# Optimization experiments

Hardware: AMD Instinct MI355X
Metric: run time of the kernel (lower is better)

The kernel has to match this reference:

```python
import jax, jax.numpy as jnp
import numpy as np

B, L, D, H, E, K = 1, 512, 512, 512, 32, 2

def setup_inputs() -> dict:
    key = jax.random.key(0)
    ks = jax.random.split(key, 6)
    x = jax.random.normal(ks[0], (B, L, D), dtype=jnp.float32)
    router_scale = 1.0 + 0.02 * jax.random.normal(ks[1], (D,), dtype=jnp.float32)
    router_logits_w = 0.02 * jax.random.normal(ks[2], (D, E), dtype=jnp.float32)
    gating_einsum = 0.02 * jax.random.normal(ks[3], (E, 2, H, D), dtype=jnp.float32)
    linear_w = 0.02 * jax.random.normal(ks[4], (E, H, D), dtype=jnp.float32)
    per_expert_scale = 1.0 + 0.02 * jax.random.normal(ks[5], (E,), dtype=jnp.float32)
    return {"x": x, "router_scale": router_scale, "router_logits_w": router_logits_w,
            "gating_einsum": gating_einsum, "linear_w": linear_w,
            "per_expert_scale": per_expert_scale}

def reference(x, router_scale, router_logits_w, gating_einsum, linear_w, per_expert_scale):
    d = x.shape[-1]
    n_experts = router_logits_w.shape[-1]
    # RMSNorm without scale (fp32)
    x32 = x.astype(jnp.float32)
    var = jnp.mean(jnp.square(x32), axis=-1, keepdims=True)
    router_input = x32 * jax.lax.rsqrt(var + 1e-6)
    root_size = jax.lax.rsqrt(jnp.asarray(d, dtype=router_input.dtype))
    router_input = router_input * root_size * router_scale.astype(router_input.dtype)
    logits = jnp.dot(router_input, router_logits_w).astype(jnp.float32)  # [B,L,E]
    probs = jax.nn.softmax(logits, axis=-1)
    _, top_k_indices = jax.lax.top_k(logits, K)  # [B,L,K]
    indicator = jax.nn.one_hot(top_k_indices, n_experts, dtype=probs.dtype).sum(axis=-2)
    gate_weights = indicator * probs
    renorm = jnp.sum(gate_weights, axis=-1, keepdims=True)
    renorm = jnp.where(renorm > 0.0, renorm, 1.0)
    weights = probs / renorm
    top_k_weights = jnp.take_along_axis(weights, top_k_indices, axis=-1)  # [B,L,K]
    output = jnp.zeros_like(x)
    for ki in range(K):  # small fixed k; faithful to source's per-slot gather
        expert_idx = top_k_indices[:, :, ki]          # [B,L] int32
        expert_w = top_k_weights[:, :, ki]            # [B,L]
        gate_params = gating_einsum[expert_idx]       # [B,L,2,H,D] -- the big gather
        lin_params = linear_w[expert_idx]             # [B,L,H,D]
        escale = per_expert_scale[expert_idx]         # [B,L]
        gate_0 = jnp.einsum('bld,blhd->blh', x, gate_params[:, :, 0])
        gate_1 = jnp.einsum('bld,blhd->blh', x, gate_params[:, :, 1])
        activated = jax.nn.gelu(gate_0) * gate_1
        expert_out = jnp.einsum('blh,blhd->bld', activated, lin_params)
        output = output + expert_out * (escale * expert_w)[..., None]
    return output
```

## Files before the change

### kernel.cpp

```cpp
#include <hip/hip_runtime.h>
#include <hip/hip_bf16.h>
#include <math.h>

#define LTOK 512
#define DDIM 512
#define NEXP 32
#define HDIM 512

typedef __attribute__((ext_vector_type(8))) short short8;
typedef __attribute__((ext_vector_type(4))) float floatx4;

__device__ __forceinline__ unsigned bpack(float a, float b) {
    unsigned ua = __float_as_uint(a), ub = __float_as_uint(b);
    ua += 0x7FFFu + ((ua >> 16) & 1u);
    ub += 0x7FFFu + ((ub >> 16) & 1u);
    return (ua >> 16) | (ub & 0xFFFF0000u);
}


__global__ __launch_bounds__(64) void router_kernel(
    const float* __restrict__ x, const float* __restrict__ rs,
    const float* __restrict__ Wr, const float* __restrict__ pes,
    int* __restrict__ easgn, float* __restrict__ wts,
    short* __restrict__ xb, float* __restrict__ out)
{
    const int t = blockIdx.x;
    const int lane = threadIdx.x;

    float xv[8];
    float ss = 0.f;
#pragma unroll
    for (int j = 0; j < 8; ++j) {
        xv[j] = x[t * DDIM + j * 64 + lane];
        ss += xv[j] * xv[j];
    }
#pragma unroll
    for (int j = 0; j < 8; ++j) {
        xb[t * DDIM + j * 64 + lane] = (short)(bpack(xv[j], 0.f) & 0xFFFFu);
        out[t * DDIM + j * 64 + lane] = 0.f;
    }

#pragma unroll
    for (int o = 32; o > 0; o >>= 1) ss += __shfl_xor(ss, o);
    const float var = ss * (1.0f / 512.0f);
    const float coef = rsqrtf(var + 1e-6f) * rsqrtf(512.0f);

    __shared__ float ri[DDIM];
#pragma unroll
    for (int j = 0; j < 8; ++j) {
        const int d = j * 64 + lane;
        ri[d] = xv[j] * coef * rs[d];
    }
    __syncthreads();

    const int e = lane & 31;
    const int half = lane >> 5;
    const int dbeg = half * 256;
    float l0 = 0.f, l1 = 0.f, l2 = 0.f, l3 = 0.f;
#pragma unroll 4
    for (int d = dbeg; d < dbeg + 256; d += 4) {
        l0 = fmaf(ri[d + 0], Wr[(d + 0) * NEXP + e], l0);
        l1 = fmaf(ri[d + 1], Wr[(d + 1) * NEXP + e], l1);
        l2 = fmaf(ri[d + 2], Wr[(d + 2) * NEXP + e], l2);
        l3 = fmaf(ri[d + 3], Wr[(d + 3) * NEXP + e], l3);
    }
    float lg = (l0 + l1) + (l2 + l3);
    lg += __shfl_xor(lg, 32);

    __shared__ float lgs[NEXP];
    if (lane < 32) lgs[lane] = lg;
    __syncthreads();

    if (lane == 0) {
        int i0 = 0; float m0 = lgs[0];
        for (int i = 1; i < NEXP; ++i) if (lgs[i] > m0) { m0 = lgs[i]; i0 = i; }
        int i1 = -1; float m1 = -1e30f;
        for (int i = 0; i < NEXP; ++i) if (i != i0 && lgs[i] > m1) { m1 = lgs[i]; i1 = i; }
        const float e1 = expf(m1 - m0);
        const float inv = 1.0f / (1.0f + e1);
        easgn[2 * t]     = i0;
        easgn[2 * t + 1] = i1;
        wts[2 * t]     = inv * pes[i0];
        wts[2 * t + 1] = e1 * inv * pes[i1];
    }
}

__global__ __launch_bounds__(256, 4) void gates_kernel(
    const short* __restrict__ xb, const float* __restrict__ G,
    const int* __restrict__ easgn, short* __restrict__ act)
{
    const int e  = blockIdx.y;
    const int h0 = blockIdx.x * 16;
    const int tid = threadIdx.x;
    const int wv   = tid >> 6;
    const int g    = wv & 1;
    const int kh   = wv >> 1;
    const int lane = tid & 63;
    const int n    = lane & 15;
    const int quad = lane >> 4;

    __shared__ int toks[2 * LTOK];
    __shared__ int lcnt;
    __shared__ float red[4][2][4][64];

    const float* Grow = G + ((size_t)((e * 2 + g) * HDIM) + h0 + n) * DDIM + kh * 256;
    const short* xbh  = xb + kh * 256;

    short8 Bf[8];
#pragma unroll
    for (int ks = 0; ks < 8; ++ks) {
        const int ko = ks * 32 + quad * 8;
        const floatx4 b0 = *(const floatx4*)(Grow + ko);
        const floatx4 b1 = *(const floatx4*)(Grow + ko + 4);
        union { short8 s; unsigned u[4]; } B;
        B.u[0] = bpack(b0.x, b0.y);
        B.u[1] = bpack(b0.z, b0.w);
        B.u[2] = bpack(b1.x, b1.y);
        B.u[3] = bpack(b1.z, b1.w);
        Bf[ks] = B.s;
    }

    if (tid == 0) lcnt = 0;
    __syncthreads();
    {
        const int4 eg = ((const int4*)easgn)[tid];
        if (eg.x == e) { int p = atomicAdd(&lcnt, 1); toks[p] = 4 * tid; }
        if (eg.y == e) { int p = atomicAdd(&lcnt, 1); toks[p] = 4 * tid + 1; }
        if (eg.z == e) { int p = atomicAdd(&lcnt, 1); toks[p] = 4 * tid + 2; }
        if (eg.w == e) { int p = atomicAdd(&lcnt, 1); toks[p] = 4 * tid + 3; }
    }
    __syncthreads();
    const int Ne = lcnt;
    if (Ne == 0) return;

    for (int mb = 0; mb < Ne; mb += 32) {
        int arow[2];
#pragma unroll
        for (int i = 0; i < 2; ++i) {
            int s = mb + i * 16 + n;
            arow[i] = toks[s < Ne ? s : Ne - 1] >> 1;
        }
        floatx4 acc[2] = {};

#pragma unroll
        for (int ks = 0; ks < 8; ++ks) {
            const int ko = ks * 32 + quad * 8;
#pragma unroll
            for (int i = 0; i < 2; ++i) {
                const short8 A = *(const short8*)(xbh + (size_t)arow[i] * DDIM + ko);
                acc[i] = __builtin_amdgcn_mfma_f32_16x16x32_bf16(A, Bf[ks], acc[i], 0, 0, 0);
            }
        }

#pragma unroll
        for (int i = 0; i < 2; ++i)
#pragma unroll
            for (int r = 0; r < 4; ++r)
                red[wv][i][r][lane] = acc[i][r];
        __syncthreads();

        {
            const int i = wv & 1;
            const int u = wv >> 1;
#pragma unroll
            for (int rr = 0; rr < 2; ++rr) {
                const int r = u * 2 + rr;
                const int s = mb + i * 16 + quad * 4 + r;
                if (s < Ne) {
                    const int a = toks[s];
                    const float g0 = red[0][i][r][lane] + red[2][i][r][lane];
                    const float g1 = red[1][i][r][lane] + red[3][i][r][lane];
                    const float uu = 0.7978845608f * (g0 + 0.044715f * g0 * g0 * g0);
                    const float sg = 1.0f / (1.0f + __expf(-2.0f * uu));
                    const float v = g0 * sg * g1;
                    act[(size_t)a * HDIM + h0 + n] = (short)(bpack(v, 0.f) & 0xFFFFu);
                }
            }
        }
        __syncthreads();
    }
}

__global__ __launch_bounds__(256, 4) void linear_kernel(
    const short* __restrict__ act, const float* __restrict__ Wl,
    const int* __restrict__ easgn, const float* __restrict__ wts,
    float* __restrict__ out)
{
    const int e  = blockIdx.y;
    const int d0 = blockIdx.x * 16;
    const int tid = threadIdx.x;
    const int wv   = tid >> 6;
    const int lane = tid & 63;
    const int n    = lane & 15;
    const int quad = lane >> 4;

    __shared__ int toks[2 * LTOK];
    __shared__ int lcnt;
    __shared__ float red[4][2][4][64];

    const float* Wcol = Wl + (size_t)e * HDIM * DDIM + d0 + n;

    short8 Bf[4];
#pragma unroll
    for (int ks = 0; ks < 4; ++ks) {
        const int ko = wv * 128 + ks * 32 + quad * 8;
        float w[8];
#pragma unroll
        for (int j = 0; j < 8; ++j)
            w[j] = Wcol[(size_t)(ko + j) * DDIM];
        union { short8 s; unsigned u[4]; } B;
        B.u[0] = bpack(w[0], w[1]);
        B.u[1] = bpack(w[2], w[3]);
        B.u[2] = bpack(w[4], w[5]);
        B.u[3] = bpack(w[6], w[7]);
        Bf[ks] = B.s;
    }

    if (tid == 0) lcnt = 0;
    __syncthreads();
    {
        const int4 eg = ((const int4*)easgn)[tid];
        if (eg.x == e) { int p = atomicAdd(&lcnt, 1); toks[p] = 4 * tid; }
        if (eg.y == e) { int p = atomicAdd(&lcnt, 1); toks[p] = 4 * tid + 1; }
        if (eg.z == e) { int p = atomicAdd(&lcnt, 1); toks[p] = 4 * tid + 2; }
        if (eg.w == e) { int p = atomicAdd(&lcnt, 1); toks[p] = 4 * tid + 3; }
    }
    __syncthreads();
    const int Ne = lcnt;
    if (Ne == 0) return;

    for (int mb = 0; mb < Ne; mb += 32) {
        int arow[2];
#pragma unroll
        for (int i = 0; i < 2; ++i) {
            int s = mb + i * 16 + n;
            arow[i] = toks[s < Ne ? s : Ne - 1];
        }
        floatx4 acc[2] = {};

#pragma unroll
        for (int ks = 0; ks < 4; ++ks) {
            const int ko = wv * 128 + ks * 32 + quad * 8;
#pragma unroll
            for (int i = 0; i < 2; ++i) {
                const short8 A = *(const short8*)(act + (size_t)arow[i] * HDIM + ko);
                acc[i] = __builtin_amdgcn_mfma_f32_16x16x32_bf16(A, Bf[ks], acc[i], 0, 0, 0);
            }
        }

#pragma unroll
        for (int i = 0; i < 2; ++i)
#pragma unroll
            for (int r = 0; r < 4; ++r)
                red[wv][i][r][lane] = acc[i][r];
        __syncthreads();

        {
            const int i = wv & 1;
            const int u = wv >> 1;
#pragma unroll
            for (int rr = 0; rr < 2; ++rr) {
                const int r = u * 2 + rr;
                const int s = mb + i * 16 + quad * 4 + r;
                if (s < Ne) {
                    const int slot = toks[s];
                    const float v = ((red[0][i][r][lane] + red[1][i][r][lane]) +
                                     (red[2][i][r][lane] + red[3][i][r][lane])) * wts[slot];
                    atomicAdd(&out[(size_t)(slot >> 1) * DDIM + d0 + n], v);
                }
            }
        }
        __syncthreads();
    }
}

extern "C" void kernel_launch(void* const* d_in, const int* in_sizes, int n_in,
                              void* d_out, int out_size, void* d_ws, size_t ws_size,
                              hipStream_t stream)
{
    const float* x   = (const float*)d_in[0];
    const float* rs  = (const float*)d_in[1];
    const float* Wr  = (const float*)d_in[2];
    const float* G   = (const float*)d_in[3];
    const float* Wl  = (const float*)d_in[4];
    const float* pes = (const float*)d_in[5];
    float* out = (float*)d_out;

    char* ws = (char*)d_ws;
    int*   easgn = (int*)(ws);
    float* wts   = (float*)(ws + 4096);
    short* xb    = (short*)(ws + 8192);
    short* act   = (short*)(ws + 532480);

    router_kernel<<<dim3(LTOK), dim3(64), 0, stream>>>(x, rs, Wr, pes, easgn, wts, xb, out);
    gates_kernel<<<dim3(32, NEXP), dim3(256), 0, stream>>>(xb, G, easgn, act);
    linear_kernel<<<dim3(32, NEXP), dim3(256), 0, stream>>>(act, Wl, easgn, wts, out);
}
```

Baseline: 158.3 us.

## Fuse router, gate and linear kernels into one persistent kernel with grid barriers

Merges the three launches into a single 1024-block kernel that uses a custom two-level atomic grid barrier between the router, gate and linear phases. Each block loads and converts both its gate and linear weight fragments to bf16 before the first barrier, so those weight loads overlap the router work instead of being serialized after each launch. The router is spread over 512 blocks of 256 threads rather than 512 blocks of 64. This relies on all 1024 blocks being co-resident (4 per CU by launch bounds); otherwise the spin barrier deadlocks. It also adds a memset launch to reset the barrier counters.

Measured after the change: 331.5 us. 2.09x slower.

```diff
diff --git a/kernel.cpp b/kernel.cpp
--- a/kernel.cpp
+++ b/kernel.cpp
@@ -17,96 +17,112 @@
     return (ua >> 16) | (ub & 0xFFFF0000u);
 }
 
-
-__global__ __launch_bounds__(64) void router_kernel(
+__device__ __forceinline__ void grid_sync(int* bar) {
+    __syncthreads();
+    if (threadIdx.x == 0) {
+        int* gcnt = bar + (int)blockIdx.y * 16;
+        int* root = bar + 512;
+        int* gen  = bar + 513;
+        const int g = __hip_atomic_load(gen, __ATOMIC_RELAXED, __HIP_MEMORY_SCOPE_AGENT);
+        __threadfence();
+        const int tgt = 32 * (g + 1) - 1;
+        const int v = __hip_atomic_fetch_add(gcnt, 1, __ATOMIC_ACQ_REL, __HIP_MEMORY_SCOPE_AGENT);
+        if (v == tgt) {
+            const int r = __hip_atomic_fetch_add(root, 1, __ATOMIC_ACQ_REL, __HIP_MEMORY_SCOPE_AGENT);
+            if (r == tgt)
+                __hip_atomic_store(gen, g + 1, __ATOMIC_RELEASE, __HIP_MEMORY_SCOPE_AGENT);
+        }
+        while (__hip_atomic_load(gen, __ATOMIC_RELAXED, __HIP_MEMORY_SCOPE_AGENT) <= g)
+            __builtin_amdgcn_s_sleep(2);
+        __threadfence();
+    }
+    __syncthreads();
+}
+
+__global__ __launch_bounds__(256, 4) void moe_fused(
     const float* __restrict__ x, const float* __restrict__ rs,
     const float* __restrict__ Wr, const float* __restrict__ pes,
-    int* __restrict__ easgn, float* __restrict__ wts,
-    short* __restrict__ xb, float* __restrict__ out)
+    const float* __restrict__ G, const float* __restrict__ Wl,
+    int* __restrict__ bar, int* __restrict__ easgn, float* __restrict__ wts,
+    short* __restrict__ xb, short* __restrict__ act, float* __restrict__ out)
 {
-    const int t = blockIdx.x;
-    const int lane = threadIdx.x;
-
-    float xv[8];
-    float ss = 0.f;
-#pragma unroll
-    for (int j = 0; j < 8; ++j) {
-        xv[j] = x[t * DDIM + j * 64 + lane];
-        ss += xv[j] * xv[j];
-    }
-#pragma unroll
-    for (int j = 0; j < 8; ++j) {
-        xb[t * DDIM + j * 64 + lane] = (short)(bpack(xv[j], 0.f) & 0xFFFFu);
-        out[t * DDIM + j * 64 + lane] = 0.f;
-    }
-
-#pragma unroll
-    for (int o = 32; o > 0; o >>= 1) ss += __shfl_xor(ss, o);
-    const float var = ss * (1.0f / 512.0f);
-    const float coef = rsqrtf(var + 1e-6f) * rsqrtf(512.0f);
-
-    __shared__ float ri[DDIM];
-#pragma unroll
-    for (int j = 0; j < 8; ++j) {
-        const int d = j * 64 + lane;
-        ri[d] = xv[j] * coef * rs[d];
-    }
-    __syncthreads();
-
-    const int e = lane & 31;
-    const int half = lane >> 5;
-    const int dbeg = half * 256;
-    float l0 = 0.f, l1 = 0.f, l2 = 0.f, l3 = 0.f;
-#pragma unroll 4
-    for (int d = dbeg; d < dbeg + 256; d += 4) {
-        l0 = fmaf(ri[d + 0], Wr[(d + 0) * NEXP + e], l0);
-        l1 = fmaf(ri[d + 1], Wr[(d + 1) * NEXP + e], l1);
-        l2 = fmaf(ri[d + 2], Wr[(d + 2) * NEXP + e], l2);
-        l3 = fmaf(ri[d + 3], Wr[(d + 3) * NEXP + e], l3);
-    }
-    float lg = (l0 + l1) + (l2 + l3);
-    lg += __shfl_xor(lg, 32);
-
-    __shared__ float lgs[NEXP];
-    if (lane < 32) lgs[lane] = lg;
-    __syncthreads();
-
-    if (lane == 0) {
-        int i0 = 0; float m0 = lgs[0];
-        for (int i = 1; i < NEXP; ++i) if (lgs[i] > m0) { m0 = lgs[i]; i0 = i; }
-        int i1 = -1; float m1 = -1e30f;
-        for (int i = 0; i < NEXP; ++i) if (i != i0 && lgs[i] > m1) { m1 = lgs[i]; i1 = i; }
-        const float e1 = expf(m1 - m0);
-        const float inv = 1.0f / (1.0f + e1);
-        easgn[2 * t]     = i0;
-        easgn[2 * t + 1] = i1;
-        wts[2 * t]     = inv * pes[i0];
-        wts[2 * t + 1] = e1 * inv * pes[i1];
-    }
-}
-
-__global__ __launch_bounds__(256, 4) void gates_kernel(
-    const short* __restrict__ xb, const float* __restrict__ G,
-    const int* __restrict__ easgn, short* __restrict__ act)
-{
-    const int e  = blockIdx.y;
-    const int h0 = blockIdx.x * 16;
-    const int tid = threadIdx.x;
+    const int tid  = threadIdx.x;
+    const int e    = blockIdx.y;
+    const int tile = blockIdx.x;
     const int wv   = tid >> 6;
-    const int g    = wv & 1;
-    const int kh   = wv >> 1;
     const int lane = tid & 63;
     const int n    = lane & 15;
     const int quad = lane >> 4;
 
-    __shared__ int toks[2 * LTOK];
-    __shared__ int lcnt;
+    __shared__ float ri[DDIM];
+    __shared__ float lgsp[8][32];
+    __shared__ float lgs[NEXP];
+    __shared__ float wsum[4];
+    __shared__ int   toks[LTOK];
+    __shared__ int   lcnt;
     __shared__ float red[4][2][4][64];
 
-    const float* Grow = G + ((size_t)((e * 2 + g) * HDIM) + h0 + n) * DDIM + kh * 256;
-    const short* xbh  = xb + kh * 256;
-
-    short8 Bf[8];
+    const int gg  = wv & 1;
+    const int kh  = wv >> 1;
+    const int t16 = tile * 16;
+    const float* Grow = G + ((size_t)((e * 2 + gg) * HDIM) + t16 + n) * DDIM + kh * 256;
+    const float* Wcol = Wl + (size_t)e * HDIM * DDIM + t16 + n;
+
+    if (tile < 16) {
+        const int t = e * 16 + tile;
+        const float2 xv = ((const float2*)(x + (size_t)t * DDIM))[tid];
+        float ss = xv.x * xv.x + xv.y * xv.y;
+#pragma unroll
+        for (int o = 32; o > 0; o >>= 1) ss += __shfl_xor(ss, o);
+        if (lane == 0) wsum[wv] = ss;
+        __syncthreads();
+        ss = (wsum[0] + wsum[1]) + (wsum[2] + wsum[3]);
+        const float coef = rsqrtf(ss * (1.0f / 512.0f) + 1e-6f) * rsqrtf(512.0f);
+
+        ((unsigned*)(xb + (size_t)t * DDIM))[tid] = bpack(xv.x, xv.y);
+        float2 z; z.x = 0.f; z.y = 0.f;
+        ((float2*)(out + (size_t)t * DDIM))[tid] = z;
+        const float2 rsv = ((const float2*)rs)[tid];
+        ri[2 * tid]     = xv.x * coef * rsv.x;
+        ri[2 * tid + 1] = xv.y * coef * rsv.y;
+        __syncthreads();
+
+        {
+            const int ee = tid & 31, seg = tid >> 5;
+            const int d0 = seg * 64;
+            float l0 = 0.f, l1 = 0.f, l2 = 0.f, l3 = 0.f;
+#pragma unroll 4
+            for (int d = d0; d < d0 + 64; d += 4) {
+                l0 = fmaf(ri[d + 0], Wr[(d + 0) * NEXP + ee], l0);
+                l1 = fmaf(ri[d + 1], Wr[(d + 1) * NEXP + ee], l1);
+                l2 = fmaf(ri[d + 2], Wr[(d + 2) * NEXP + ee], l2);
+                l3 = fmaf(ri[d + 3], Wr[(d + 3) * NEXP + ee], l3);
+            }
+            lgsp[seg][ee] = (l0 + l1) + (l2 + l3);
+        }
+        __syncthreads();
+        if (tid < 32) {
+            float lg = 0.f;
+#pragma unroll
+            for (int s = 0; s < 8; ++s) lg += lgsp[s][tid];
+            lgs[tid] = lg;
+        }
+        __syncthreads();
+        if (tid == 0) {
+            int i0 = 0; float m0 = lgs[0];
+            for (int i = 1; i < NEXP; ++i) if (lgs[i] > m0) { m0 = lgs[i]; i0 = i; }
+            int i1 = -1; float m1 = -1e30f;
+            for (int i = 0; i < NEXP; ++i) if (i != i0 && lgs[i] > m1) { m1 = lgs[i]; i1 = i; }
+            const float e1 = expf(m1 - m0);
+            const float inv = 1.0f / (1.0f + e1);
+            easgn[2 * t]     = i0;
+            easgn[2 * t + 1] = i1;
+            wts[2 * t]     = inv * pes[i0];
+            wts[2 * t + 1] = e1 * inv * pes[i1];
+        }
+    }
+
+    short8 Bg[8];
 #pragma unroll
     for (int ks = 0; ks < 8; ++ks) {
         const int ko = ks * 32 + quad * 8;
@@ -117,90 +133,9 @@
         B.u[1] = bpack(b0.z, b0.w);
         B.u[2] = bpack(b1.x, b1.y);
         B.u[3] = bpack(b1.z, b1.w);
-        Bf[ks] = B.s;
-    }
-
-    if (tid == 0) lcnt = 0;
-    __syncthreads();
-    {
-        const int4 eg = ((const int4*)easgn)[tid];
-        if (eg.x == e) { int p = atomicAdd(&lcnt, 1); toks[p] = 4 * tid; }
-        if (eg.y == e) { int p = atomicAdd(&lcnt, 1); toks[p] = 4 * tid + 1; }
-        if (eg.z == e) { int p = atomicAdd(&lcnt, 1); toks[p] = 4 * tid + 2; }
-        if (eg.w == e) { int p = atomicAdd(&lcnt, 1); toks[p] = 4 * tid + 3; }
-    }
-    __syncthreads();
-    const int Ne = lcnt;
-    if (Ne == 0) return;
-
-    for (int mb = 0; mb < Ne; mb += 32) {
-        int arow[2];
-#pragma unroll
-        for (int i = 0; i < 2; ++i) {
-            int s = mb + i * 16 + n;
-            arow[i] = toks[s < Ne ? s : Ne - 1] >> 1;
-        }
-        floatx4 acc[2] = {};
-
-#pragma unroll
-        for (int ks = 0; ks < 8; ++ks) {
-            const int ko = ks * 32 + quad * 8;
-#pragma unroll
-            for (int i = 0; i < 2; ++i) {
-                const short8 A = *(const short8*)(xbh + (size_t)arow[i] * DDIM + ko);
-                acc[i] = __builtin_amdgcn_mfma_f32_16x16x32_bf16(A, Bf[ks], acc[i], 0, 0, 0);
-            }
-        }
-
-#pragma unroll
-        for (int i = 0; i < 2; ++i)
-#pragma unroll
-            for (int r = 0; r < 4; ++r)
-                red[wv][i][r][lane] = acc[i][r];
-        __syncthreads();
-
-        {
-            const int i = wv & 1;
-            const int u = wv >> 1;
-#pragma unroll
-            for (int rr = 0; rr < 2; ++rr) {
-                const int r = u * 2 + rr;
-                const int s = mb + i * 16 + quad * 4 + r;
-                if (s < Ne) {
-                    const int a = toks[s];
-                    const float g0 = red[0][i][r][lane] + red[2][i][r][lane];
-                    const float g1 = red[1][i][r][lane] + red[3][i][r][lane];
-                    const float uu = 0.7978845608f * (g0 + 0.044715f * g0 * g0 * g0);
-                    const float sg = 1.0f / (1.0f + __expf(-2.0f * uu));
-                    const float v = g0 * sg * g1;
-                    act[(size_t)a * HDIM + h0 + n] = (short)(bpack(v, 0.f) & 0xFFFFu);
-                }
-            }
-        }
-        __syncthreads();
-    }
-}
-
-__global__ __launch_bounds__(256, 4) void linear_kernel(
-    const short* __restrict__ act, const float* __restrict__ Wl,
-    const int* __restrict__ easgn, const float* __restrict__ wts,
-    float* __restrict__ out)
-{
-    const int e  = blockIdx.y;
-    const int d0 = blockIdx.x * 16;
-    const int tid = threadIdx.x;
-    const int wv   = tid >> 6;
-    const int lane = tid & 63;
-    const int n    = lane & 15;
-    const int quad = lane >> 4;
-
-    __shared__ int toks[2 * LTOK];
-    __shared__ int lcnt;
-    __shared__ float red[4][2][4][64];
-
-    const float* Wcol = Wl + (size_t)e * HDIM * DDIM + d0 + n;
-
-    short8 Bf[4];
+        Bg[ks] = B.s;
+    }
+    short8 Bl[4];
 #pragma unroll
     for (int ks = 0; ks < 4; ++ks) {
         const int ko = wv * 128 + ks * 32 + quad * 8;
@@ -213,8 +148,10 @@
         B.u[1] = bpack(w[2], w[3]);
         B.u[2] = bpack(w[4], w[5]);
         B.u[3] = bpack(w[6], w[7]);
-        Bf[ks] = B.s;
-    }
+        Bl[ks] = B.s;
+    }
+
+    grid_sync(bar);
 
     if (tid == 0) lcnt = 0;
     __syncthreads();
@@ -227,50 +164,97 @@
     }
     __syncthreads();
     const int Ne = lcnt;
-    if (Ne == 0) return;
-
-    for (int mb = 0; mb < Ne; mb += 32) {
-        int arow[2];
-#pragma unroll
-        for (int i = 0; i < 2; ++i) {
-            int s = mb + i * 16 + n;
-            arow[i] = toks[s < Ne ? s : Ne - 1];
-        }
-        floatx4 acc[2] = {};
-
-#pragma unroll
-        for (int ks = 0; ks < 4; ++ks) {
-            const int ko = wv * 128 + ks * 32 + quad * 8;
+
+    if (Ne > 0) {
+        const short* xbh = xb + kh * 256;
+        for (int mb = 0; mb < Ne; mb += 32) {
+            int arow[2];
 #pragma unroll
             for (int i = 0; i < 2; ++i) {
-                const short8 A = *(const short8*)(act + (size_t)arow[i] * HDIM + ko);
-                acc[i] = __builtin_amdgcn_mfma_f32_16x16x32_bf16(A, Bf[ks], acc[i], 0, 0, 0);
-            }
-        }
-
-#pragma unroll
-        for (int i = 0; i < 2; ++i)
-#pragma unroll
-            for (int r = 0; r < 4; ++r)
-                red[wv][i][r][lane] = acc[i][r];
-        __syncthreads();
-
-        {
-            const int i = wv & 1;
-            const int u = wv >> 1;
-#pragma unroll
-            for (int rr = 0; rr < 2; ++rr) {
-                const int r = u * 2 + rr;
-                const int s = mb + i * 16 + quad * 4 + r;
-                if (s < Ne) {
-                    const int slot = toks[s];
-                    const float v = ((red[0][i][r][lane] + red[1][i][r][lane]) +
-                                     (red[2][i][r][lane] + red[3][i][r][lane])) * wts[slot];
-                    atomicAdd(&out[(size_t)(slot >> 1) * DDIM + d0 + n], v);
-                }
-            }
-        }
-        __syncthreads();
+                int s = mb + i * 16 + n;
+                arow[i] = toks[s < Ne ? s : Ne - 1] >> 1;
+            }
+            floatx4 acc[2] = {};
+#pragma unroll
+            for (int ks = 0; ks < 8; ++ks) {
+                const int ko = ks * 32 + quad * 8;
+#pragma unroll
+                for (int i = 0; i < 2; ++i) {
+                    const short8 A = *(const short8*)(xbh + (size_t)arow[i] * DDIM + ko);
+                    acc[i] = __builtin_amdgcn_mfma_f32_16x16x32_bf16(A, Bg[ks], acc[i], 0, 0, 0);
+                }
+            }
+#pragma unroll
+            for (int i = 0; i < 2; ++i)
+#pragma unroll
+                for (int r = 0; r < 4; ++r)
+                    red[wv][i][r][lane] = acc[i][r];
+            __syncthreads();
+            {
+                const int i = wv & 1;
+                const int u = wv >> 1;
+#pragma unroll
+                for (int rr = 0; rr < 2; ++rr) {
+                    const int r = u * 2 + rr;
+                    const int s = mb + i * 16 + quad * 4 + r;
+                    if (s < Ne) {
+                        const int a = toks[s];
+                        const float g0 = red[0][i][r][lane] + red[2][i][r][lane];
+                        const float g1 = red[1][i][r][lane] + red[3][i][r][lane];
+                        const float uu = 0.7978845608f * (g0 + 0.044715f * g0 * g0 * g0);
+                        const float sg = 1.0f / (1.0f + __expf(-2.0f * uu));
+                        const float v = g0 * sg * g1;
+                        act[(size_t)a * HDIM + t16 + n] = (short)(bpack(v, 0.f) & 0xFFFFu);
+                    }
+                }
+            }
+            __syncthreads();
+        }
+    }
+
+    grid_sync(bar);
+
+    if (Ne > 0) {
+        for (int mb = 0; mb < Ne; mb += 32) {
+            int arow[2];
+#pragma unroll
+            for (int i = 0; i < 2; ++i) {
+                int s = mb + i * 16 + n;
+                arow[i] = toks[s < Ne ? s : Ne - 1];
+            }
+            floatx4 acc[2] = {};
+#pragma unroll
+            for (int ks = 0; ks < 4; ++ks) {
+                const int ko = wv * 128 + ks * 32 + quad * 8;
+#pragma unroll
+                for (int i = 0; i < 2; ++i) {
+                    const short8 A = *(const short8*)(act + (size_t)arow[i] * HDIM + ko);
+                    acc[i] = __builtin_amdgcn_mfma_f32_16x16x32_bf16(A, Bl[ks], acc[i], 0, 0, 0);
+                }
+            }
+#pragma unroll
+            for (int i = 0; i < 2; ++i)
+#pragma unroll
+                for (int r = 0; r < 4; ++r)
+                    red[wv][i][r][lane] = acc[i][r];
+            __syncthreads();
+            {
+                const int i = wv & 1;
+                const int u = wv >> 1;
+#pragma unroll
+                for (int rr = 0; rr < 2; ++rr) {
+                    const int r = u * 2 + rr;
+                    const int s = mb + i * 16 + quad * 4 + r;
+                    if (s < Ne) {
+                        const int slot = toks[s];
+                        const float v = ((red[0][i][r][lane] + red[1][i][r][lane]) +
+                                         (red[2][i][r][lane] + red[3][i][r][lane])) * wts[slot];
+                        atomicAdd(&out[(size_t)(slot >> 1) * DDIM + t16 + n], v);
+                    }
+                }
+            }
+            __syncthreads();
+        }
     }
 }
 
@@ -287,12 +271,13 @@
     float* out = (float*)d_out;
 
     char* ws = (char*)d_ws;
-    int*   easgn = (int*)(ws);
-    float* wts   = (float*)(ws + 4096);
-    short* xb    = (short*)(ws + 8192);
-    short* act   = (short*)(ws + 532480);
-
-    router_kernel<<<dim3(LTOK), dim3(64), 0, stream>>>(x, rs, Wr, pes, easgn, wts, xb, out);
-    gates_kernel<<<dim3(32, NEXP), dim3(256), 0, stream>>>(xb, G, easgn, act);
-    linear_kernel<<<dim3(32, NEXP), dim3(256), 0, stream>>>(act, Wl, easgn, wts, out);
-}
+    int*   bar   = (int*)(ws);
+    int*   easgn = (int*)(ws + 4096);
+    float* wts   = (float*)(ws + 8192);
+    short* xb    = (short*)(ws + 12288);
+    short* act   = (short*)(ws + 536576);
+
+    hipMemsetAsync(bar, 0, 4096, stream);
+    moe_fused<<<dim3(32, 32), dim3(256), 0, stream>>>(
+        x, rs, Wr, pes, G, Wl, bar, easgn, wts, xb, act, out);
+}
```

## Fuse gate and linear expert kernels with shared-memory activation window

Applied to the files above, without the earlier changes.

Merges the gate-projection and down-projection kernels into one expert kernel. Each block computes GELU-gated activations for 32 hidden units, stages them in shared memory, and immediately multiplies by the matching slice of the linear weights, accumulating into the output with atomics. This removes the global activation buffer and one kernel launch. In exchange, every block does a partial hidden-dim reduction, so output atomics increase and register pressure rises, which is why occupancy is lowered to 2 blocks.

Result: slower. 168.1 us (+6.2%).

```diff
diff --git a/kernel.cpp b/kernel.cpp
--- a/kernel.cpp
+++ b/kernel.cpp
@@ -85,12 +85,13 @@
     }
 }
 
-__global__ __launch_bounds__(256, 4) void gates_kernel(
+__global__ __launch_bounds__(256, 2) void expert_kernel(
     const short* __restrict__ xb, const float* __restrict__ G,
-    const int* __restrict__ easgn, short* __restrict__ act)
+    const float* __restrict__ Wl, const int* __restrict__ easgn,
+    const float* __restrict__ wts, float* __restrict__ out)
 {
     const int e  = blockIdx.y;
-    const int h0 = blockIdx.x * 16;
+    const int h0 = blockIdx.x * 32;
     const int tid = threadIdx.x;
     const int wv   = tid >> 6;
     const int g    = wv & 1;
@@ -99,174 +100,119 @@
     const int n    = lane & 15;
     const int quad = lane >> 4;
 
-    __shared__ int toks[2 * LTOK];
-    __shared__ int lcnt;
-    __shared__ float red[4][2][4][64];
-
-    const float* Grow = G + ((size_t)((e * 2 + g) * HDIM) + h0 + n) * DDIM + kh * 256;
-    const short* xbh  = xb + kh * 256;
-
-    short8 Bf[8];
-#pragma unroll
-    for (int ks = 0; ks < 8; ++ks) {
-        const int ko = ks * 32 + quad * 8;
-        const floatx4 b0 = *(const floatx4*)(Grow + ko);
-        const floatx4 b1 = *(const floatx4*)(Grow + ko + 4);
-        union { short8 s; unsigned u[4]; } B;
-        B.u[0] = bpack(b0.x, b0.y);
-        B.u[1] = bpack(b0.z, b0.w);
-        B.u[2] = bpack(b1.x, b1.y);
-        B.u[3] = bpack(b1.z, b1.w);
-        Bf[ks] = B.s;
-    }
-
-    if (tid == 0) lcnt = 0;
-    __syncthreads();
-    {
-        const int4 eg = ((const int4*)easgn)[tid];
-        if (eg.x == e) { int p = atomicAdd(&lcnt, 1); toks[p] = 4 * tid; }
-        if (eg.y == e) { int p = atomicAdd(&lcnt, 1); toks[p] = 4 * tid + 1; }
-        if (eg.z == e) { int p = atomicAdd(&lcnt, 1); toks[p] = 4 * tid + 2; }
-        if (eg.w == e) { int p = atomicAdd(&lcnt, 1); toks[p] = 4 * tid + 3; }
-    }
-    __syncthreads();
-    const int Ne = lcnt;
-    if (Ne == 0) return;
-
-    for (int mb = 0; mb < Ne; mb += 32) {
-        int arow[2];
-#pragma unroll
-        for (int i = 0; i < 2; ++i) {
-            int s = mb + i * 16 + n;
-            arow[i] = toks[s < Ne ? s : Ne - 1] >> 1;
-        }
-        floatx4 acc[2] = {};
-
+    __shared__ int   toks[LTOK];
+    __shared__ float wsl[LTOK];
+    __shared__ int   lcnt;
+    __shared__ float red[4][2][2][4][64];
+    __shared__ __align__(16) short act_win[32][40];
+
+    short8 Bg[2][8];
+#pragma unroll
+    for (int nt = 0; nt < 2; ++nt) {
+        const float* Grow = G + ((size_t)((e * 2 + g) * HDIM) + h0 + nt * 16 + n) * DDIM + kh * 256;
 #pragma unroll
         for (int ks = 0; ks < 8; ++ks) {
             const int ko = ks * 32 + quad * 8;
-#pragma unroll
-            for (int i = 0; i < 2; ++i) {
-                const short8 A = *(const short8*)(xbh + (size_t)arow[i] * DDIM + ko);
-                acc[i] = __builtin_amdgcn_mfma_f32_16x16x32_bf16(A, Bf[ks], acc[i], 0, 0, 0);
-            }
-        }
-
-#pragma unroll
-        for (int i = 0; i < 2; ++i)
-#pragma unroll
-            for (int r = 0; r < 4; ++r)
-                red[wv][i][r][lane] = acc[i][r];
-        __syncthreads();
-
-        {
-            const int i = wv & 1;
-            const int u = wv >> 1;
-#pragma unroll
-            for (int rr = 0; rr < 2; ++rr) {
-                const int r = u * 2 + rr;
-                const int s = mb + i * 16 + quad * 4 + r;
-                if (s < Ne) {
-                    const int a = toks[s];
-                    const float g0 = red[0][i][r][lane] + red[2][i][r][lane];
-                    const float g1 = red[1][i][r][lane] + red[3][i][r][lane];
-                    const float uu = 0.7978845608f * (g0 + 0.044715f * g0 * g0 * g0);
-                    const float sg = 1.0f / (1.0f + __expf(-2.0f * uu));
-                    const float v = g0 * sg * g1;
-                    act[(size_t)a * HDIM + h0 + n] = (short)(bpack(v, 0.f) & 0xFFFFu);
-                }
-            }
-        }
-        __syncthreads();
-    }
-}
-
-__global__ __launch_bounds__(256, 4) void linear_kernel(
-    const short* __restrict__ act, const float* __restrict__ Wl,
-    const int* __restrict__ easgn, const float* __restrict__ wts,
-    float* __restrict__ out)
-{
-    const int e  = blockIdx.y;
-    const int d0 = blockIdx.x * 16;
-    const int tid = threadIdx.x;
-    const int wv   = tid >> 6;
-    const int lane = tid & 63;
-    const int n    = lane & 15;
-    const int quad = lane >> 4;
-
-    __shared__ int toks[2 * LTOK];
-    __shared__ int lcnt;
-    __shared__ float red[4][2][4][64];
-
-    const float* Wcol = Wl + (size_t)e * HDIM * DDIM + d0 + n;
-
-    short8 Bf[4];
-#pragma unroll
-    for (int ks = 0; ks < 4; ++ks) {
-        const int ko = wv * 128 + ks * 32 + quad * 8;
+            const floatx4 b0 = *(const floatx4*)(Grow + ko);
+            const floatx4 b1 = *(const floatx4*)(Grow + ko + 4);
+            union { short8 s; unsigned u[4]; } B;
+            B.u[0] = bpack(b0.x, b0.y);
+            B.u[1] = bpack(b0.z, b0.w);
+            B.u[2] = bpack(b1.x, b1.y);
+            B.u[3] = bpack(b1.z, b1.w);
+            Bg[nt][ks] = B.s;
+        }
+    }
+    short8 Bl[8];
+#pragma unroll
+    for (int nt2 = 0; nt2 < 8; ++nt2) {
+        const float* Wcol = Wl + ((size_t)e * HDIM + h0 + quad * 8) * DDIM + wv * 128 + nt2 * 16 + n;
         float w[8];
 #pragma unroll
         for (int j = 0; j < 8; ++j)
-            w[j] = Wcol[(size_t)(ko + j) * DDIM];
+            w[j] = Wcol[(size_t)j * DDIM];
         union { short8 s; unsigned u[4]; } B;
         B.u[0] = bpack(w[0], w[1]);
         B.u[1] = bpack(w[2], w[3]);
         B.u[2] = bpack(w[4], w[5]);
         B.u[3] = bpack(w[6], w[7]);
-        Bf[ks] = B.s;
+        Bl[nt2] = B.s;
     }
 
     if (tid == 0) lcnt = 0;
     __syncthreads();
     {
         const int4 eg = ((const int4*)easgn)[tid];
-        if (eg.x == e) { int p = atomicAdd(&lcnt, 1); toks[p] = 4 * tid; }
-        if (eg.y == e) { int p = atomicAdd(&lcnt, 1); toks[p] = 4 * tid + 1; }
-        if (eg.z == e) { int p = atomicAdd(&lcnt, 1); toks[p] = 4 * tid + 2; }
-        if (eg.w == e) { int p = atomicAdd(&lcnt, 1); toks[p] = 4 * tid + 3; }
+        if (eg.x == e) { int p = atomicAdd(&lcnt, 1); toks[p] = 4 * tid;     wsl[p] = wts[4 * tid]; }
+        if (eg.y == e) { int p = atomicAdd(&lcnt, 1); toks[p] = 4 * tid + 1; wsl[p] = wts[4 * tid + 1]; }
+        if (eg.z == e) { int p = atomicAdd(&lcnt, 1); toks[p] = 4 * tid + 2; wsl[p] = wts[4 * tid + 2]; }
+        if (eg.w == e) { int p = atomicAdd(&lcnt, 1); toks[p] = 4 * tid + 3; wsl[p] = wts[4 * tid + 3]; }
     }
     __syncthreads();
     const int Ne = lcnt;
     if (Ne == 0) return;
 
+    const short* xbh = xb + kh * 256;
+
     for (int mb = 0; mb < Ne; mb += 32) {
         int arow[2];
 #pragma unroll
         for (int i = 0; i < 2; ++i) {
             int s = mb + i * 16 + n;
-            arow[i] = toks[s < Ne ? s : Ne - 1];
-        }
-        floatx4 acc[2] = {};
-
-#pragma unroll
-        for (int ks = 0; ks < 4; ++ks) {
-            const int ko = wv * 128 + ks * 32 + quad * 8;
+            arow[i] = toks[s < Ne ? s : Ne - 1] >> 1;
+        }
+
+        floatx4 acc[2][2] = {};
+#pragma unroll
+        for (int ks = 0; ks < 8; ++ks) {
+            const int ko = ks * 32 + quad * 8;
 #pragma unroll
             for (int i = 0; i < 2; ++i) {
-                const short8 A = *(const short8*)(act + (size_t)arow[i] * HDIM + ko);
-                acc[i] = __builtin_amdgcn_mfma_f32_16x16x32_bf16(A, Bf[ks], acc[i], 0, 0, 0);
+                const short8 A = *(const short8*)(xbh + (size_t)arow[i] * DDIM + ko);
+#pragma unroll
+                for (int nt = 0; nt < 2; ++nt)
+                    acc[i][nt] = __builtin_amdgcn_mfma_f32_16x16x32_bf16(A, Bg[nt][ks], acc[i][nt], 0, 0, 0);
             }
         }
-
 #pragma unroll
         for (int i = 0; i < 2; ++i)
 #pragma unroll
-            for (int r = 0; r < 4; ++r)
-                red[wv][i][r][lane] = acc[i][r];
+            for (int nt = 0; nt < 2; ++nt)
+#pragma unroll
+                for (int r = 0; r < 4; ++r)
+                    red[wv][i][nt][r][lane] = acc[i][nt][r];
         __syncthreads();
 
         {
-            const int i = wv & 1;
-            const int u = wv >> 1;
-#pragma unroll
-            for (int rr = 0; rr < 2; ++rr) {
-                const int r = u * 2 + rr;
-                const int s = mb + i * 16 + quad * 4 + r;
+            const int m  = wv & 1;
+            const int nt = wv >> 1;
+#pragma unroll
+            for (int r = 0; r < 4; ++r) {
+                const int s = mb + m * 16 + quad * 4 + r;
                 if (s < Ne) {
-                    const int slot = toks[s];
-                    const float v = ((red[0][i][r][lane] + red[1][i][r][lane]) +
-                                     (red[2][i][r][lane] + red[3][i][r][lane])) * wts[slot];
-                    atomicAdd(&out[(size_t)(slot >> 1) * DDIM + d0 + n], v);
+                    const float g0 = red[0][m][nt][r][lane] + red[2][m][nt][r][lane];
+                    const float g1 = red[1][m][nt][r][lane] + red[3][m][nt][r][lane];
+                    const float uu = 0.7978845608f * (g0 + 0.044715f * g0 * g0 * g0);
+                    const float sg = 1.0f / (1.0f + __expf(-2.0f * uu));
+                    const float v = g0 * sg * g1 * wsl[s];
+                    act_win[m * 16 + quad * 4 + r][nt * 16 + n] = (short)(bpack(v, 0.f) & 0xFFFFu);
+                }
+            }
+        }
+        __syncthreads();
+
+#pragma unroll
+        for (int i = 0; i < 2; ++i) {
+            const short8 Aw = *(const short8*)&act_win[i * 16 + n][quad * 8];
+#pragma unroll
+            for (int nt2 = 0; nt2 < 8; ++nt2) {
+                floatx4 y = {};
+                y = __builtin_amdgcn_mfma_f32_16x16x32_bf16(Aw, Bl[nt2], y, 0, 0, 0);
+#pragma unroll
+                for (int r = 0; r < 4; ++r) {
+                    const int s = mb + i * 16 + quad * 4 + r;
+                    if (s < Ne)
+                        atomicAdd(&out[(size_t)(toks[s] >> 1) * DDIM + wv * 128 + nt2 * 16 + n], y[r]);
                 }
             }
         }
@@ -290,9 +236,7 @@
     int*   easgn = (int*)(ws);
     float* wts   = (float*)(ws + 4096);
     short* xb    = (short*)(ws + 8192);
-    short* act   = (short*)(ws + 532480);
 
     router_kernel<<<dim3(LTOK), dim3(64), 0, stream>>>(x, rs, Wr, pes, easgn, wts, xb, out);
-    gates_kernel<<<dim3(32, NEXP), dim3(256), 0, stream>>>(xb, G, easgn, act);
-    linear_kernel<<<dim3(32, NEXP), dim3(256), 0, stream>>>(act, Wl, easgn, wts, out);
-}
+    expert_kernel<<<dim3(16, NEXP), dim3(256), 0, stream>>>(xb, G, Wl, easgn, wts, out);
+}
```
